# Kernel tuning notes

Hardware: AMD Instinct MI355X
Metric: run time of the kernel (lower is better)

Reference implementation:

```python
import jax, jax.numpy as jnp
import numpy as np

# irreps_in = 128x0e + 64x1o + 32x2e -> (multiplicity, 2l+1) blocks
IRREPS = [(128, 1), (64, 3), (32, 5)]
DIM = sum(m * d for m, d in IRREPS)  # 480
EPS = 1e-8


def setup_inputs() -> dict:
    key = jax.random.key(0)
    features = jax.random.normal(key, (100000, DIM), dtype=jnp.float32)
    return {"features": features}


def reference(features) -> jnp.ndarray:
    batch = features.shape[:-1]
    out_blocks = []
    off = 0
    for mul, d in IRREPS:  # fixed small structural loop over irrep types
        block = features[..., off:off + mul * d].reshape(*batch, mul, d)
        # per-irrep L2 norm over the (2l+1) components -> (..., mul)
        norms = jnp.sqrt(jnp.sum(block * block, axis=-1))
        eps_norms = jnp.maximum(norms, EPS)
        scalings = jax.nn.silu(eps_norms) / eps_norms
        out_blocks.append((block * scalings[..., None]).reshape(*batch, mul * d))
        off += mul * d
    return jnp.concatenate(out_blocks, axis=-1)
```

## Files before the change

### kernel.cpp

```cpp
#include <hip/hip_runtime.h>
#include <math.h>

#define ROWS_PER_BLOCK 8
#define DIM 480
#define NGROUPS 224
#define NV4 120
#define BLOCK 256

__global__ __launch_bounds__(BLOCK) void norm_act_kernel(
    const float* __restrict__ in, float* __restrict__ out, int n_rows)
{
    __shared__ float sdata[ROWS_PER_BLOCK * DIM];
    __shared__ float sscal[ROWS_PER_BLOCK * NGROUPS];

    const int tid  = threadIdx.x;
    const int row0 = blockIdx.x * ROWS_PER_BLOCK;
    const int rows = min(ROWS_PER_BLOCK, n_rows - row0);
    const int nv4  = rows * NV4;

    const float4* gin  = (const float4*)(in  + (size_t)row0 * DIM);
    float4*       gout = (float4*)      (out + (size_t)row0 * DIM);

    for (int v = tid; v < nv4; v += BLOCK) {
        ((float4*)sdata)[v] = gin[v];
    }
    __syncthreads();

    const int ng = rows * NGROUPS;
    for (int g = tid; g < ng; g += BLOCK) {
        const int row = g / NGROUPS;
        const int gi  = g - row * NGROUPS;
        const float* base = sdata + row * DIM;
        float ss;
        if (gi < 128) {
            const float x = base[gi];
            ss = x * x;
        } else if (gi < 192) {
            const float* p = base + 128 + (gi - 128) * 3;
            ss = p[0]*p[0] + p[1]*p[1] + p[2]*p[2];
        } else {
            const float* p = base + 320 + (gi - 192) * 5;
            ss = p[0]*p[0] + p[1]*p[1] + p[2]*p[2] + p[3]*p[3] + p[4]*p[4];
        }
        float n = sqrtf(ss);
        n = fmaxf(n, 1e-8f);
        sscal[row * NGROUPS + gi] = 1.0f / (1.0f + __expf(-n));
    }
    __syncthreads();

    for (int v = tid; v < nv4; v += BLOCK) {
        const int row = v / NV4;
        const int c4  = v - row * NV4;
        const int e0  = c4 * 4;
        float4 x = ((const float4*)sdata)[v];
        const float* sc = sscal + row * NGROUPS;
        float s[4];
        #pragma unroll
        for (int k = 0; k < 4; ++k) {
            const int e = e0 + k;
            int gidx;
            if (e < 128)       gidx = e;
            else if (e < 320)  gidx = 128 + (e - 128) / 3;
            else               gidx = 192 + (e - 320) / 5;
            s[k] = sc[gidx];
        }
        x.x *= s[0]; x.y *= s[1]; x.z *= s[2]; x.w *= s[3];
        gout[v] = x;
    }
}

extern "C" void kernel_launch(void* const* d_in, const int* in_sizes, int n_in,
                              void* d_out, int out_size, void* d_ws, size_t ws_size,
                              hipStream_t stream) {
    const float* in  = (const float*)d_in[0];
    float*       out = (float*)d_out;
    const int n_rows = in_sizes[0] / DIM;
    const int grid   = (n_rows + ROWS_PER_BLOCK - 1) / ROWS_PER_BLOCK;
    norm_act_kernel<<<grid, BLOCK, 0, stream>>>(in, out, n_rows);
}
```

Measured before the change: 322.2 us.

## Replace shared-memory staging with per-thread register processing of whole irrep groups

Drops the LDS staging, the two __syncthreads barriers and the group-index lookup. Each thread now loads whole groups of four irreps straight from global memory with float4 loads, computes their norms and scales in registers, and writes them back. Threads are split into three ranges by irrep type. This should cut LDS traffic and the div/mod cost, but the l=1 and l=2 threads make strided multi-float4 accesses that coalesce less well across a wavefront. Some wavefronts that straddle range boundaries may also diverge.

```diff
diff --git a/kernel.cpp b/kernel.cpp
--- a/kernel.cpp
+++ b/kernel.cpp
@@ -1,71 +1,65 @@
 #include <hip/hip_runtime.h>
 #include <math.h>
 
-#define ROWS_PER_BLOCK 8
 #define DIM 480
-#define NGROUPS 224
-#define NV4 120
 #define BLOCK 256
 
+__device__ __forceinline__ float sig_scale(float ss) {
+    float n = fmaxf(sqrtf(ss), 1e-8f);
+    return 1.0f / (1.0f + __expf(-n));
+}
+
 __global__ __launch_bounds__(BLOCK) void norm_act_kernel(
-    const float* __restrict__ in, float* __restrict__ out, int n_rows)
+    const float* __restrict__ in, float* __restrict__ out,
+    int nA, int nAB, int total)
 {
-    __shared__ float sdata[ROWS_PER_BLOCK * DIM];
-    __shared__ float sscal[ROWS_PER_BLOCK * NGROUPS];
+    const int t = blockIdx.x * BLOCK + threadIdx.x;
+    if (t >= total) return;
 
-    const int tid  = threadIdx.x;
-    const int row0 = blockIdx.x * ROWS_PER_BLOCK;
-    const int rows = min(ROWS_PER_BLOCK, n_rows - row0);
-    const int nv4  = rows * NV4;
-
-    const float4* gin  = (const float4*)(in  + (size_t)row0 * DIM);
-    float4*       gout = (float4*)      (out + (size_t)row0 * DIM);
-
-    for (int v = tid; v < nv4; v += BLOCK) {
-        ((float4*)sdata)[v] = gin[v];
-    }
-    __syncthreads();
-
-    const int ng = rows * NGROUPS;
-    for (int g = tid; g < ng; g += BLOCK) {
-        const int row = g / NGROUPS;
-        const int gi  = g - row * NGROUPS;
-        const float* base = sdata + row * DIM;
-        float ss;
-        if (gi < 128) {
-            const float x = base[gi];
-            ss = x * x;
-        } else if (gi < 192) {
-            const float* p = base + 128 + (gi - 128) * 3;
-            ss = p[0]*p[0] + p[1]*p[1] + p[2]*p[2];
-        } else {
-            const float* p = base + 320 + (gi - 192) * 5;
-            ss = p[0]*p[0] + p[1]*p[1] + p[2]*p[2] + p[3]*p[3] + p[4]*p[4];
-        }
-        float n = sqrtf(ss);
-        n = fmaxf(n, 1e-8f);
-        sscal[row * NGROUPS + gi] = 1.0f / (1.0f + __expf(-n));
-    }
-    __syncthreads();
-
-    for (int v = tid; v < nv4; v += BLOCK) {
-        const int row = v / NV4;
-        const int c4  = v - row * NV4;
-        const int e0  = c4 * 4;
-        float4 x = ((const float4*)sdata)[v];
-        const float* sc = sscal + row * NGROUPS;
-        float s[4];
-        #pragma unroll
-        for (int k = 0; k < 4; ++k) {
-            const int e = e0 + k;
-            int gidx;
-            if (e < 128)       gidx = e;
-            else if (e < 320)  gidx = 128 + (e - 128) / 3;
-            else               gidx = 192 + (e - 320) / 5;
-            s[k] = sc[gidx];
-        }
-        x.x *= s[0]; x.y *= s[1]; x.z *= s[2]; x.w *= s[3];
-        gout[v] = x;
+    if (t < nA) {
+        const int row = t >> 5;
+        const int ci  = t & 31;
+        const size_t off = (size_t)row * DIM + (size_t)ci * 4;
+        float4 x = *(const float4*)(in + off);
+        x.x *= sig_scale(x.x * x.x);
+        x.y *= sig_scale(x.y * x.y);
+        x.z *= sig_scale(x.z * x.z);
+        x.w *= sig_scale(x.w * x.w);
+        *(float4*)(out + off) = x;
+    } else if (t < nAB) {
+        const int i   = t - nA;
+        const int row = i >> 4;
+        const int ci  = i & 15;
+        const size_t off = (size_t)row * DIM + 128 + (size_t)ci * 12;
+        const float4* p = (const float4*)(in + off);
+        float4 a = p[0], b = p[1], c = p[2];
+        const float s0 = sig_scale(a.x*a.x + a.y*a.y + a.z*a.z);
+        const float s1 = sig_scale(a.w*a.w + b.x*b.x + b.y*b.y);
+        const float s2 = sig_scale(b.z*b.z + b.w*b.w + c.x*c.x);
+        const float s3 = sig_scale(c.y*c.y + c.z*c.z + c.w*c.w);
+        a.x *= s0; a.y *= s0; a.z *= s0; a.w *= s1;
+        b.x *= s1; b.y *= s1; b.z *= s2; b.w *= s2;
+        c.x *= s2; c.y *= s3; c.z *= s3; c.w *= s3;
+        float4* q = (float4*)(out + off);
+        q[0] = a; q[1] = b; q[2] = c;
+    } else {
+        const int i   = t - nAB;
+        const int row = i >> 3;
+        const int ci  = i & 7;
+        const size_t off = (size_t)row * DIM + 320 + (size_t)ci * 20;
+        const float4* p = (const float4*)(in + off);
+        float4 a = p[0], b = p[1], c = p[2], d = p[3], e = p[4];
+        const float s0 = sig_scale(a.x*a.x + a.y*a.y + a.z*a.z + a.w*a.w + b.x*b.x);
+        const float s1 = sig_scale(b.y*b.y + b.z*b.z + b.w*b.w + c.x*c.x + c.y*c.y);
+        const float s2 = sig_scale(c.z*c.z + c.w*c.w + d.x*d.x + d.y*d.y + d.z*d.z);
+        const float s3 = sig_scale(d.w*d.w + e.x*e.x + e.y*e.y + e.z*e.z + e.w*e.w);
+        a.x *= s0; a.y *= s0; a.z *= s0; a.w *= s0;
+        b.x *= s0; b.y *= s1; b.z *= s1; b.w *= s1;
+        c.x *= s1; c.y *= s1; c.z *= s2; c.w *= s2;
+        d.x *= s2; d.y *= s2; d.z *= s2; d.w *= s3;
+        e.x *= s3; e.y *= s3; e.z *= s3; e.w *= s3;
+        float4* q = (float4*)(out + off);
+        q[0] = a; q[1] = b; q[2] = c; q[3] = d; q[4] = e;
     }
 }
 
@@ -75,6 +69,9 @@
     const float* in  = (const float*)d_in[0];
     float*       out = (float*)d_out;
     const int n_rows = in_sizes[0] / DIM;
-    const int grid   = (n_rows + ROWS_PER_BLOCK - 1) / ROWS_PER_BLOCK;
-    norm_act_kernel<<<grid, BLOCK, 0, stream>>>(in, out, n_rows);
+    const int nA     = n_rows * 32;
+    const int nAB    = nA + n_rows * 16;
+    const int total  = nAB + n_rows * 8;
+    const int grid   = (total + BLOCK - 1) / BLOCK;
+    norm_act_kernel<<<grid, BLOCK, 0, stream>>>(in, out, nA, nAB, total);
 }
```

Measured after the change: 331.7 us. 1.03x slower.

## Use single-wave blocks with direct global-to-LDS loads and in-place scaling

Applied to the files above, without the earlier changes.

Restructures the kernel so each block is one 64-lane wavefront handling 8 rows. Rows are loaded into LDS with global_load_lds and the per-group sigmoid scaling is applied in place, which removes the separate scale array, the per-element group-index division and the block-wide barriers. The sigmoid reciprocal becomes a hardware rcp approximation. The risks are lower per-block parallelism, since 64 threads now cover 8 rows, and the correctness of the LDS address mapping for the direct-to-LDS load.

```diff
diff --git a/kernel.cpp b/kernel.cpp
--- a/kernel.cpp
+++ b/kernel.cpp
@@ -1,71 +1,98 @@
 #include <hip/hip_runtime.h>
 #include <math.h>
 
-#define ROWS_PER_BLOCK 8
 #define DIM 480
-#define NGROUPS 224
-#define NV4 120
-#define BLOCK 256
+#define ROWS 8
+#define BLOCK 64
+#define NLOADS 15
+
+__device__ __forceinline__ float sig_of(float n) {
+    n = fmaxf(n, 1e-8f);
+    return __builtin_amdgcn_rcpf(1.0f + __expf(-n));
+}
+
+template <int R>
+__device__ __forceinline__ void scale_groups(float* sbuf, int lane) {
+    #pragma unroll
+    for (int k = 0; k < R * 2; ++k) {
+        const int a = k * 64 + lane;
+        float* p = sbuf + (a >> 7) * DIM + (a & 127);
+        const float x = *p;
+        *p = x * sig_of(fabsf(x));
+    }
+    #pragma unroll
+    for (int k = 0; k < R; ++k) {
+        const int b = k * 64 + lane;
+        float* p = sbuf + (b >> 6) * DIM + 128 + 3 * (b & 63);
+        const float x0 = p[0], x1 = p[1], x2 = p[2];
+        const float s = sig_of(sqrtf(x0*x0 + x1*x1 + x2*x2));
+        p[0] = x0 * s; p[1] = x1 * s; p[2] = x2 * s;
+    }
+    #pragma unroll
+    for (int k = 0; k < R / 2; ++k) {
+        const int c = k * 64 + lane;
+        float* p = sbuf + (c >> 5) * DIM + 320 + 5 * (c & 31);
+        const float x0 = p[0], x1 = p[1], x2 = p[2], x3 = p[3], x4 = p[4];
+        const float s = sig_of(sqrtf(x0*x0 + x1*x1 + x2*x2 + x3*x3 + x4*x4));
+        p[0] = x0*s; p[1] = x1*s; p[2] = x2*s; p[3] = x3*s; p[4] = x4*s;
+    }
+}
+
+__device__ void scale_groups_rt(float* sbuf, int lane, int rows) {
+    for (int a = lane; a < rows * 128; a += 64) {
+        float* p = sbuf + (a >> 7) * DIM + (a & 127);
+        const float x = *p;
+        *p = x * sig_of(fabsf(x));
+    }
+    for (int b = lane; b < rows * 64; b += 64) {
+        float* p = sbuf + (b >> 6) * DIM + 128 + 3 * (b & 63);
+        const float x0 = p[0], x1 = p[1], x2 = p[2];
+        const float s = sig_of(sqrtf(x0*x0 + x1*x1 + x2*x2));
+        p[0] = x0 * s; p[1] = x1 * s; p[2] = x2 * s;
+    }
+    for (int c = lane; c < rows * 32; c += 64) {
+        float* p = sbuf + (c >> 5) * DIM + 320 + 5 * (c & 31);
+        const float x0 = p[0], x1 = p[1], x2 = p[2], x3 = p[3], x4 = p[4];
+        const float s = sig_of(sqrtf(x0*x0 + x1*x1 + x2*x2 + x3*x3 + x4*x4));
+        p[0] = x0*s; p[1] = x1*s; p[2] = x2*s; p[3] = x3*s; p[4] = x4*s;
+    }
+}
 
 __global__ __launch_bounds__(BLOCK) void norm_act_kernel(
     const float* __restrict__ in, float* __restrict__ out, int n_rows)
 {
-    __shared__ float sdata[ROWS_PER_BLOCK * DIM];
-    __shared__ float sscal[ROWS_PER_BLOCK * NGROUPS];
+    __shared__ __align__(16) float sbuf[ROWS * DIM];
+    const int lane = threadIdx.x;
+    const int row0 = blockIdx.x * ROWS;
+    const int rows = min(ROWS, n_rows - row0);
 
-    const int tid  = threadIdx.x;
-    const int row0 = blockIdx.x * ROWS_PER_BLOCK;
-    const int rows = min(ROWS_PER_BLOCK, n_rows - row0);
-    const int nv4  = rows * NV4;
+    const float* gsrc = in  + (size_t)row0 * DIM;
+    float*       gdst = out + (size_t)row0 * DIM;
 
-    const float4* gin  = (const float4*)(in  + (size_t)row0 * DIM);
-    float4*       gout = (float4*)      (out + (size_t)row0 * DIM);
+    if (rows == ROWS) {
+        #pragma unroll
+        for (int k = 0; k < NLOADS; ++k) {
+            const float* gp = gsrc + (size_t)(k * 64 + lane) * 4;
+            __builtin_amdgcn_global_load_lds(
+                (const __attribute__((address_space(1))) void*)gp,
+                (__attribute__((address_space(3))) void*)((char*)sbuf + k * 1024),
+                16, 0, 0);
+        }
+        asm volatile("s_waitcnt vmcnt(0)" ::: "memory");
 
-    for (int v = tid; v < nv4; v += BLOCK) {
-        ((float4*)sdata)[v] = gin[v];
-    }
-    __syncthreads();
+        scale_groups<ROWS>(sbuf, lane);
 
-    const int ng = rows * NGROUPS;
-    for (int g = tid; g < ng; g += BLOCK) {
-        const int row = g / NGROUPS;
-        const int gi  = g - row * NGROUPS;
-        const float* base = sdata + row * DIM;
-        float ss;
-        if (gi < 128) {
-            const float x = base[gi];
-            ss = x * x;
-        } else if (gi < 192) {
-            const float* p = base + 128 + (gi - 128) * 3;
-            ss = p[0]*p[0] + p[1]*p[1] + p[2]*p[2];
-        } else {
-            const float* p = base + 320 + (gi - 192) * 5;
-            ss = p[0]*p[0] + p[1]*p[1] + p[2]*p[2] + p[3]*p[3] + p[4]*p[4];
+        #pragma unroll
+        for (int k = 0; k < NLOADS; ++k) {
+            const int v = k * 64 + lane;
+            ((float4*)gdst)[v] = ((const float4*)sbuf)[v];
         }
-        float n = sqrtf(ss);
-        n = fmaxf(n, 1e-8f);
-        sscal[row * NGROUPS + gi] = 1.0f / (1.0f + __expf(-n));
-    }
-    __syncthreads();
-
-    for (int v = tid; v < nv4; v += BLOCK) {
-        const int row = v / NV4;
-        const int c4  = v - row * NV4;
-        const int e0  = c4 * 4;
-        float4 x = ((const float4*)sdata)[v];
-        const float* sc = sscal + row * NGROUPS;
-        float s[4];
-        #pragma unroll
-        for (int k = 0; k < 4; ++k) {
-            const int e = e0 + k;
-            int gidx;
-            if (e < 128)       gidx = e;
-            else if (e < 320)  gidx = 128 + (e - 128) / 3;
-            else               gidx = 192 + (e - 320) / 5;
-            s[k] = sc[gidx];
-        }
-        x.x *= s[0]; x.y *= s[1]; x.z *= s[2]; x.w *= s[3];
-        gout[v] = x;
+    } else if (rows > 0) {
+        for (int v = lane; v < rows * (DIM / 4); v += BLOCK)
+            ((float4*)sbuf)[v] = ((const float4*)gsrc)[v];
+        scale_groups_rt(sbuf, lane, rows);
+        for (int v = lane; v < rows * (DIM / 4); v += BLOCK)
+            ((float4*)gdst)[v] = ((const float4*)sbuf)[v];
     }
 }
 
@@ -75,6 +102,6 @@
     const float* in  = (const float*)d_in[0];
     float*       out = (float*)d_out;
     const int n_rows = in_sizes[0] / DIM;
-    const int grid   = (n_rows + ROWS_PER_BLOCK - 1) / ROWS_PER_BLOCK;
+    const int grid   = (n_rows + ROWS - 1) / ROWS;
     norm_act_kernel<<<grid, BLOCK, 0, stream>>>(in, out, n_rows);
 }
```

New measurement: 319.2 us. About the same (-0.9%).

## Replace LDS-staged row blocks with per-irrep wavefront tasks using lane shuffles

Applied to the files above, without the earlier changes.

Drops shared-memory staging and the two block barriers. Work is split into wavefront-sized tasks per irrep type, and float4 lanes compute group norms via cross-lane shuffles. The launch becomes a fixed-size grid-stride loop with nontemporal stores and a fast reciprocal. Some lanes idle in the l=1 and l=2 sections, and the index math is more complex.

```diff
diff --git a/kernel.cpp b/kernel.cpp
--- a/kernel.cpp
+++ b/kernel.cpp
@@ -1,71 +1,95 @@
 #include <hip/hip_runtime.h>
 #include <math.h>
 
-#define ROWS_PER_BLOCK 8
 #define DIM 480
-#define NGROUPS 224
-#define NV4 120
 #define BLOCK 256
+#define NBLOCKS 2048
+
+typedef float f4 __attribute__((ext_vector_type(4)));
+
+__device__ __forceinline__ float sig_of(float n) {
+    n = fmaxf(n, 1e-8f);
+    return __builtin_amdgcn_rcpf(1.0f + __expf(-n));
+}
 
 __global__ __launch_bounds__(BLOCK) void norm_act_kernel(
     const float* __restrict__ in, float* __restrict__ out, int n_rows)
 {
-    __shared__ float sdata[ROWS_PER_BLOCK * DIM];
-    __shared__ float sscal[ROWS_PER_BLOCK * NGROUPS];
+    const int l  = threadIdx.x & 63;
+    const int gw = blockIdx.x * (BLOCK / 64) + (threadIdx.x >> 6);
+    const int ws = gridDim.x * (BLOCK / 64);
 
-    const int tid  = threadIdx.x;
-    const int row0 = blockIdx.x * ROWS_PER_BLOCK;
-    const int rows = min(ROWS_PER_BLOCK, n_rows - row0);
-    const int nv4  = rows * NV4;
+    const f4* gin  = (const f4*)in;
+    f4*       gout = (f4*)out;
 
-    const float4* gin  = (const float4*)(in  + (size_t)row0 * DIM);
-    float4*       gout = (float4*)      (out + (size_t)row0 * DIM);
+    const int nA4 = n_rows * 32;
+    const int NB  = n_rows * 16;
+    const int NC  = n_rows * 8;
+    const int WA  = (nA4 + 63) >> 6;
+    const int WB  = (NB + 20) / 21;
+    const int WC  = (NC + 11) / 12;
+    const int WT  = WA + WB + WC;
 
-    for (int v = tid; v < nv4; v += BLOCK) {
-        ((float4*)sdata)[v] = gin[v];
-    }
-    __syncthreads();
-
-    const int ng = rows * NGROUPS;
-    for (int g = tid; g < ng; g += BLOCK) {
-        const int row = g / NGROUPS;
-        const int gi  = g - row * NGROUPS;
-        const float* base = sdata + row * DIM;
-        float ss;
-        if (gi < 128) {
-            const float x = base[gi];
-            ss = x * x;
-        } else if (gi < 192) {
-            const float* p = base + 128 + (gi - 128) * 3;
-            ss = p[0]*p[0] + p[1]*p[1] + p[2]*p[2];
+    for (int w = gw; w < WT; w += ws) {
+        if (w < WA) {
+            const int a = (w << 6) + l;
+            if (a < nA4) {
+                const size_t j = (size_t)(a >> 5) * 120 + (a & 31);
+                f4 x = gin[j];
+                x.x *= sig_of(fabsf(x.x));
+                x.y *= sig_of(fabsf(x.y));
+                x.z *= sig_of(fabsf(x.z));
+                x.w *= sig_of(fabsf(x.w));
+                __builtin_nontemporal_store(x, gout + j);
+            }
+        } else if (w < WA + WB) {
+            const int cl = l / 3;
+            const int p  = l - cl * 3;
+            const int c  = (w - WA) * 21 + cl;
+            const bool act = (l < 63) && (c < NB);
+            const size_t j = (size_t)(c >> 4) * 120 + 32 + 3 * (c & 15) + p;
+            f4 x = {0.f, 0.f, 0.f, 0.f};
+            if (act) x = gin[j];
+            const float q0 = x.x*x.x, q1 = x.y*x.y, q2 = x.z*x.z, q3 = x.w*x.w;
+            const float lo = q0 + (p < 2 ? q1 : 0.f) + (p == 0 ? q2 : 0.f);
+            const float hi = q3 + (p > 0 ? q2 : 0.f) + (p == 2 ? q1 : 0.f);
+            const float prev_hi = __shfl(hi, (l - 1) & 63);
+            const float next_lo = __shfl(lo, (l + 1) & 63);
+            const float gA = lo + (p == 0 ? 0.f : prev_hi);
+            const float gB = hi + (p == 2 ? 0.f : next_lo);
+            const float sA = sig_of(sqrtf(gA));
+            const float sB = sig_of(sqrtf(gB));
+            x.x *= sA;
+            x.y *= (p < 2)  ? sA : sB;
+            x.z *= (p == 0) ? sA : sB;
+            x.w *= sB;
+            if (act) __builtin_nontemporal_store(x, gout + j);
         } else {
-            const float* p = base + 320 + (gi - 192) * 5;
-            ss = p[0]*p[0] + p[1]*p[1] + p[2]*p[2] + p[3]*p[3] + p[4]*p[4];
+            const int cl = l / 5;
+            const int p  = l - cl * 5;
+            const int c  = (w - WA - WB) * 12 + cl;
+            const bool act = (l < 60) && (c < NC);
+            const size_t j = (size_t)(c >> 3) * 120 + 80 + 5 * (c & 7) + p;
+            f4 x = {0.f, 0.f, 0.f, 0.f};
+            if (act) x = gin[j];
+            const float q0 = x.x*x.x, q1 = x.y*x.y, q2 = x.z*x.z, q3 = x.w*x.w;
+            const int t = (p == 0 || p == 4) ? 4 : p;
+            const float lo = q0 + (t > 1 ? q1 : 0.f) + (t > 2 ? q2 : 0.f)
+                                + (t > 3 ? q3 : 0.f);
+            const float hi = (q0 + q1 + q2 + q3) - lo;
+            const float prev_lo = __shfl(lo, (l - 1) & 63);
+            const float prev_hi = __shfl(hi, (l - 1) & 63);
+            const float next_lo = __shfl(lo, (l + 1) & 63);
+            const float gA = lo + (p == 0 ? next_lo : (p == 1 ? prev_lo : prev_hi));
+            const float gB = (p == 0 || p == 4) ? gA : hi + next_lo;
+            const float sA = sig_of(sqrtf(gA));
+            const float sB = sig_of(sqrtf(gB));
+            x.x *= sA;
+            x.y *= (t > 1) ? sA : sB;
+            x.z *= (t > 2) ? sA : sB;
+            x.w *= (t > 3) ? sA : sB;
+            if (act) __builtin_nontemporal_store(x, gout + j);
         }
-        float n = sqrtf(ss);
-        n = fmaxf(n, 1e-8f);
-        sscal[row * NGROUPS + gi] = 1.0f / (1.0f + __expf(-n));
-    }
-    __syncthreads();
-
-    for (int v = tid; v < nv4; v += BLOCK) {
-        const int row = v / NV4;
-        const int c4  = v - row * NV4;
-        const int e0  = c4 * 4;
-        float4 x = ((const float4*)sdata)[v];
-        const float* sc = sscal + row * NGROUPS;
-        float s[4];
-        #pragma unroll
-        for (int k = 0; k < 4; ++k) {
-            const int e = e0 + k;
-            int gidx;
-            if (e < 128)       gidx = e;
-            else if (e < 320)  gidx = 128 + (e - 128) / 3;
-            else               gidx = 192 + (e - 320) / 5;
-            s[k] = sc[gidx];
-        }
-        x.x *= s[0]; x.y *= s[1]; x.z *= s[2]; x.w *= s[3];
-        gout[v] = x;
     }
 }
 
@@ -75,6 +99,5 @@
     const float* in  = (const float*)d_in[0];
     float*       out = (float*)d_out;
     const int n_rows = in_sizes[0] / DIM;
-    const int grid   = (n_rows + ROWS_PER_BLOCK - 1) / ROWS_PER_BLOCK;
-    norm_act_kernel<<<grid, BLOCK, 0, stream>>>(in, out, n_rows);
+    norm_act_kernel<<<NBLOCKS, BLOCK, 0, stream>>>(in, out, n_rows);
 }
```

Measured after the change: 333.0 us. +3.4%, slower.
